# Optimization experiments

Hardware: AMD Instinct MI355X
Metric: run time of the kernel (lower is better)

## Reference

```python
import jax, jax.numpy as jnp
import numpy as np

M1 = M2 = 16      # spectral modes
CM1 = CM2 = 4     # cft modes = modes // 4
L_SEG = 4
M_CHEB = 8
PAD = 9


def _cft2d(x):
    # x: [B,C,H,W]; H,W divisible by L_SEG, segment length divisible by M_CHEB
    B, C, H, W = x.shape
    hs, ws = H // L_SEG, W // L_SEG
    seg = x.reshape(B, C, L_SEG, hs, L_SEG, ws).transpose(0, 1, 2, 4, 3, 5)
    seg = seg.reshape(B, C, L_SEG * L_SEG, hs * ws)  # row-major segment order (i,j)
    seg = seg / jnp.maximum(jnp.linalg.norm(seg, axis=-1, keepdims=True), 1e-12)
    # torch x[:,:,k::M].mean over k=0..M-1 == reshape (n//M, M), mean over rows
    coeffs = seg.reshape(B, C, L_SEG * L_SEG, (hs * ws) // M_CHEB, M_CHEB).mean(axis=3)
    coeffs = coeffs.reshape(B, C, -1)[:, :, : CM1 * CM2]
    return coeffs.reshape(B, C, CM1, CM2)  # real part; imag part is zero


def _spectral_rc(x, w1, w2, g1w, g1b, g2w, g2b):
    B, C, H, W = x.shape
    xft = jnp.fft.rfft2(x, axes=(-2, -1))
    top = jnp.einsum('bixy,ioxy->boxy', xft[:, :, :M1, :M2], w1)
    bot = jnp.einsum('bixy,ioxy->boxy', xft[:, :, H - M1:, :M2], w2)
    out_ft = jnp.zeros((B, w1.shape[1], H, W // 2 + 1), dtype=xft.dtype)
    out_ft = out_ft.at[:, :, :M1, :M2].set(top)
    out_ft = out_ft.at[:, :, H - M1:, :M2].set(bot)
    x_fno = jnp.fft.irfft2(out_ft, s=(H, W), axes=(-2, -1))
    cr = _cft2d(x)
    # torch.view_as_real interleaves (real, imag) on last axis; imag == 0
    cflat = jnp.stack([cr, jnp.zeros_like(cr)], axis=-1).reshape(B, -1)
    h = jax.nn.gelu(cflat @ g1w.T + g1b, approximate=False)
    corr = h @ g2w.T + g2b  # [B, C_out]
    return x_fno + corr[:, :, None, None]


def _forward(x, sw1r, sw1i, sw2r, sw2i, g1w, g1b, g2w, g2b, cw, cb,
             fc0w, fc0b, fc1w, fc1b, fc2w, fc2b):
    B, S1, S2, _ = x.shape
    gx = jnp.broadcast_to(jnp.linspace(0., 1., S1, dtype=x.dtype)[None, :, None, None], (B, S1, S2, 1))
    gy = jnp.broadcast_to(jnp.linspace(0., 1., S2, dtype=x.dtype)[None, None, :, None], (B, S1, S2, 1))
    h = jnp.concatenate([x, gx, gy], axis=-1) @ fc0w.T + fc0b
    h = h.transpose(0, 3, 1, 2)
    h = jnp.pad(h, ((0, 0), (0, 0), (0, PAD), (0, PAD)))
    for l in range(4):
        w1 = sw1r[l] + 1j * sw1i[l]
        w2 = sw2r[l] + 1j * sw2i[l]
        h1 = _spectral_rc(h, w1, w2, g1w[l], g1b[l], g2w[l], g2b[l])
        h2 = jnp.einsum('bchw,oc->bohw', h, cw[l]) + cb[l][None, :, None, None]
        h = h1 + h2
        if l < 3:
            h = jax.nn.gelu(h, approximate=False)
    h = h[..., :-PAD, :-PAD].transpose(0, 2, 3, 1)
    h = jax.nn.gelu(h @ fc1w.T + fc1b, approximate=False)
    return h @ fc2w.T + fc2b


def setup_inputs():
    key = jax.random.key(0)
    ks = jax.random.split(key, 20)
    B, S, Cin, Cout, Wd = 8, 119, 3, 1, 64
    f32 = jnp.float32
    scale = 1.0 / (Wd * Wd)
    return {
        'x': jax.random.normal(ks[0], (B, S, S, Cin), f32),
        'sw1r': scale * jax.random.uniform(ks[1], (4, Wd, Wd, M1, M2), f32),
        'sw1i': scale * jax.random.uniform(ks[2], (4, Wd, Wd, M1, M2), f32),
        'sw2r': scale * jax.random.uniform(ks[3], (4, Wd, Wd, M1, M2), f32),
        'sw2i': scale * jax.random.uniform(ks[4], (4, Wd, Wd, M1, M2), f32),
        'g1w': 0.02 * jax.random.normal(ks[5], (4, 256, 2048), f32),
        'g1b': 0.02 * jax.random.normal(ks[6], (4, 256), f32),
        'g2w': 0.02 * jax.random.normal(ks[7], (4, Wd, 256), f32),
        'g2b': 0.02 * jax.random.normal(ks[8], (4, Wd), f32),
        'cw': (1.0 / 8.0) * jax.random.normal(ks[9], (4, Wd, Wd), f32),
        'cb': 0.1 * jax.random.normal(ks[10], (4, Wd), f32),
        'fc0w': 0.4 * jax.random.normal(ks[11], (Wd, Cin + 2), f32),
        'fc0b': 0.1 * jax.random.normal(ks[12], (Wd,), f32),
        'fc1w': (1.0 / 8.0) * jax.random.normal(ks[13], (128, Wd), f32),
        'fc1b': 0.1 * jax.random.normal(ks[14], (128,), f32),
        'fc2w': (1.0 / 11.3) * jax.random.normal(ks[15], (Cout, 128), f32),
        'fc2b': 0.1 * jax.random.normal(ks[16], (Cout,), f32),
    }


def reference(x, sw1r, sw1i, sw2r, sw2i, g1w, g1b, g2w, g2b, cw, cb,
              fc0w, fc0b, fc1w, fc1b, fc2w, fc2b):
    return _forward(x, sw1r, sw1i, sw2r, sw2i, g1w, g1b, g2w, g2b, cw, cb,
                    fc0w, fc0b, fc1w, fc1b, fc2w, fc2b)
```

## Files before the change

### kernel.cpp

```cpp
#include <hip/hip_runtime.h>
#include <math.h>

#define NB 8
#define NC 64
#define NH 128
#define NW 128
#define NS 119
#define NPIX 113288

__device__ __forceinline__ float gelu_f(float v) {
    return 0.5f * v * (1.0f + erff(v * 0.70710678118654752f));
}

__global__ void __launch_bounds__(128) k_trig(float2* __restrict__ trig) {
    int t = threadIdx.x;
    double a = (double)t * (3.14159265358979323846 / 64.0);
    trig[t] = make_float2((float)cos(a), (float)sin(a));
}

__global__ void __launch_bounds__(128) k_tab(float2* __restrict__ wd) {
    int idx = blockIdx.x * 128 + threadIdx.x;
    int ky = idx >> 7, w = idx & 127;
    int prod = (ky * w) & 127;
    double a = (double)prod * (3.14159265358979323846 / 64.0);
    wd[idx] = make_float2((float)cos(a), (float)(-sin(a)));
}

__global__ void __launch_bounds__(256) k_tc(const float* __restrict__ fc1w,
                                            const float* __restrict__ cw,
                                            float* __restrict__ fc1wT,
                                            float* __restrict__ cwT) {
    int u = blockIdx.x * 256 + threadIdx.x;
    if (u < 8192) {
        int c = u >> 7, j = u & 127;
        fc1wT[u] = fc1w[j * 64 + c];
    } else {
        int v = u - 8192;
        int l = v >> 12, idx = v & 4095;
        int c = idx >> 6, o = idx & 63;
        cwT[v] = cw[l * 4096 + o * 64 + c];
    }
}

__global__ void __launch_bounds__(256) k_fc0(const float* __restrict__ x,
                                             const float* __restrict__ w,
                                             const float* __restrict__ bia,
                                             float* __restrict__ h) {
    __shared__ float sw[320];
    __shared__ float sb[64];
    int t = threadIdx.x;
    for (int u = t; u < 320; u += 256) sw[u] = w[u];
    if (t < 64) sb[t] = bia[t];
    __syncthreads();
    int p = blockIdx.x * 256 + t;
    int b = p >> 14;
    int rem = p & 16383;
    int r = rem >> 7, wc = rem & 127;
    float v0 = 0.f, v1 = 0.f, v2 = 0.f, gx = 0.f, gy = 0.f;
    bool inside = (r < NS) && (wc < NS);
    if (inside) {
        const float* xp = x + ((size_t)(b * NS + r) * NS + wc) * 3;
        v0 = xp[0]; v1 = xp[1]; v2 = xp[2];
        gx = (float)r * (1.0f / 118.0f);
        gy = (float)wc * (1.0f / 118.0f);
    }
    float* hp = h + (size_t)b * NC * NH * NW + rem;
    for (int c = 0; c < 64; ++c) {
        float val = 0.f;
        if (inside) {
            const float* wr = sw + c * 5;
            val = v0 * wr[0] + v1 * wr[1] + v2 * wr[2] + gx * wr[3] + gy * wr[4] + sb[c];
        }
        hp[c * (NH * NW)] = val;
    }
}

__global__ void __launch_bounds__(256) k_dft2(const float* __restrict__ h,
                                              float2* __restrict__ xft,
                                              float* __restrict__ cr,
                                              const float2* __restrict__ wd,
                                              const float2* __restrict__ trig) {
    __shared__ __align__(16) float sx[32][132];
    __shared__ __align__(16) float2 sW[16][134];
    __shared__ float2 sT[128][17];
    __shared__ float2 st[128];
    __shared__ float s_cs[2][32][8];
    __shared__ float s_cq[2][32][8];
    int t = threadIdx.x;
    int bc = blockIdx.x;
    if (t < 128) st[t] = trig[t];
    for (int u = t; u < 2048; u += 256) sW[u >> 7][u & 127] = wd[u];
    const float* src = h + (size_t)bc * 16384;
    int rp = t >> 4, ky = t & 15;
    for (int it = 0; it < 4; ++it) {
        __syncthreads();
        for (int u = t; u < 4096; u += 256) sx[u >> 7][u & 127] = src[it * 4096 + u];
        __syncthreads();
        const float* xa = sx[2 * rp];
        const float* xb = sx[2 * rp + 1];
        const float2* wk = sW[ky];
        float rea = 0.f, ima = 0.f, reb = 0.f, imb = 0.f;
#pragma unroll 8
        for (int w0 = 0; w0 < 128; w0 += 4) {
            float4 a4 = *(const float4*)(xa + w0);
            float4 b4 = *(const float4*)(xb + w0);
            float4 w01 = *(const float4*)(wk + w0);
            float4 w23 = *(const float4*)(wk + w0 + 2);
            rea += a4.x * w01.x; ima += a4.x * w01.y;
            reb += b4.x * w01.x; imb += b4.x * w01.y;
            rea += a4.y * w01.z; ima += a4.y * w01.w;
            reb += b4.y * w01.z; imb += b4.y * w01.w;
            rea += a4.z * w23.x; ima += a4.z * w23.y;
            reb += b4.z * w23.x; imb += b4.z * w23.y;
            rea += a4.w * w23.z; ima += a4.w * w23.w;
            reb += b4.w * w23.z; imb += b4.w * w23.w;
        }
        sT[it * 32 + 2 * rp][ky] = make_float2(rea, ima);
        sT[it * 32 + 2 * rp + 1][ky] = make_float2(reb, imb);
        if (it == 0) {
            int rr = t >> 3, k = t & 7;
            const float* row = sx[rr];
            float cs0 = 0.f, cq0 = 0.f, cs1 = 0.f, cq1 = 0.f;
#pragma unroll
            for (int g = 0; g < 4; ++g) {
                float a = row[g * 8 + k];       cs0 += a;  cq0 += a * a;
                float bv = row[32 + g * 8 + k]; cs1 += bv; cq1 += bv * bv;
            }
            s_cs[0][rr][k] = cs0; s_cs[1][rr][k] = cs1;
            s_cq[0][rr][k] = cq0; s_cq[1][rr][k] = cq1;
        }
    }
    __syncthreads();
    int mlo = t >> 4;
    int kxa = mlo, kxb = 112 + mlo;
    float2 sva = st[kxa]; float sca = sva.x, ssa = -sva.y;
    float2 svb = st[kxb]; float scb = svb.x, ssb = -svb.y;
    float rea = 0.f, ima = 0.f, reb = 0.f, imb = 0.f;
    for (int h0 = 0; h0 < 128; h0 += 16) {
        float2 bva = st[(kxa * h0) & 127]; float cca = bva.x, csa = -bva.y;
        float2 bvb = st[(kxb * h0) & 127]; float ccb = bvb.x, csb = -bvb.y;
#pragma unroll
        for (int j = 0; j < 16; ++j) {
            float2 Tv = sT[h0 + j][ky];
            rea += Tv.x * cca - Tv.y * csa;
            ima += Tv.x * csa + Tv.y * cca;
            reb += Tv.x * ccb - Tv.y * csb;
            imb += Tv.x * csb + Tv.y * ccb;
            float na = cca * sca - csa * ssa; csa = cca * ssa + csa * sca; cca = na;
            float nb = ccb * scb - csb * ssb; csb = ccb * ssb + csb * scb; ccb = nb;
        }
    }
    float2* xp = xft + (size_t)bc * 512;
    xp[mlo * 16 + ky] = make_float2(rea, ima);
    xp[(mlo + 16) * 16 + ky] = make_float2(reb, imb);
    if (t < 16) {
        int half = t >> 3, k = t & 7;
        float s = 0.f, q = 0.f;
        for (int rr = 0; rr < 32; ++rr) {
            s += s_cs[half][rr][k];
#pragma unroll
            for (int kk = 0; kk < 8; ++kk) q += s_cq[half][rr][kk];
        }
        float norm = fmaxf(sqrtf(q), 1e-12f);
        cr[bc * 16 + t] = s / (128.0f * norm);
    }
}

__global__ void __launch_bounds__(512) k_mixmlp(const float2* __restrict__ xft,
                                                const float* __restrict__ w1r,
                                                const float* __restrict__ w1i,
                                                const float* __restrict__ w2r,
                                                const float* __restrict__ w2i,
                                                const float* __restrict__ cr,
                                                const float* __restrict__ g1w,
                                                const float* __restrict__ g1b,
                                                float* __restrict__ hmid,
                                                float2* __restrict__ F) {
    __shared__ __align__(16) char smem[36864];
    int t = threadIdx.x;
    int bid = blockIdx.x;
    if (bid < 512) {
        float2* s_w = (float2*)smem;
        float2* s_x = (float2*)(smem + 32768);
        int m = (bid & 7) + 8 * ((bid >> 3) & 3);
        int e = bid >> 5;
        const float* wr; const float* wi; int mm;
        if (m < 16) { wr = w1r; wi = w1i; mm = m; } else { wr = w2r; wi = w2i; mm = m - 16; }
        int off = mm * 16 + e;
        for (int u = t; u < 4096; u += 512) {
            s_w[u] = make_float2(wr[(u << 8) + off], wi[(u << 8) + off]);
        }
        {
            int bb = t >> 6, i = t & 63;
            s_x[bb * 64 + i] = xft[((size_t)(bb * 64 + i) * 32 + m) * 16 + e];
        }
        __syncthreads();
        int bb = t >> 6, o = t & 63;
        float re = 0.f, im = 0.f;
#pragma unroll 8
        for (int i = 0; i < 64; ++i) {
            float2 xv = s_x[bb * 64 + i];
            float2 wv = s_w[i * 64 + o];
            re += xv.x * wv.x - xv.y * wv.y;
            im += xv.x * wv.y + xv.y * wv.x;
        }
        F[((size_t)(bb * 16 + e) * 32 + m) * 64 + o] = make_float2(re, im);
    } else {
        float* s_cr   = (float*)smem;
        float* s_wave = (float*)(smem + 32768);
        int j = bid - 512;
        for (int u = t; u < 8192; u += 512) s_cr[u] = cr[u];
        const float* wrow = g1w + (size_t)j * 2048;
        float w0 = wrow[4 * t], w1 = wrow[4 * t + 2];
        __syncthreads();
        float acc[8];
#pragma unroll
        for (int b = 0; b < 8; ++b) {
            float2 v = *(const float2*)(s_cr + b * 1024 + 2 * t);
            acc[b] = v.x * w0 + v.y * w1;
        }
#pragma unroll
        for (int d = 32; d > 0; d >>= 1) {
#pragma unroll
            for (int b = 0; b < 8; ++b) acc[b] += __shfl_down(acc[b], d, 64);
        }
        int wv = t >> 6;
        if ((t & 63) == 0) {
#pragma unroll
            for (int b = 0; b < 8; ++b) s_wave[wv * 8 + b] = acc[b];
        }
        __syncthreads();
        if (t < 8) {
            float a = g1b[j];
            for (int q = 0; q < 8; ++q) a += s_wave[q * 8 + t];
            hmid[t * 256 + j] = gelu_f(a);
        }
    }
}

__global__ void __launch_bounds__(256, 4) k_invb(const float2* __restrict__ F,
                                                 const float* __restrict__ hin,
                                                 const float* __restrict__ cwTl,
                                                 const float* __restrict__ cbl,
                                                 const float* __restrict__ hmid,
                                                 const float* __restrict__ g2w,
                                                 const float* __restrict__ g2b,
                                                 const float2* __restrict__ trig,
                                                 float* __restrict__ hout,
                                                 int do_gelu) {
    int blk = blockIdx.x;
    int b = blk >> 7, h = blk & 127;
    __shared__ __align__(16) float s_cwT[64][64];
    __shared__ __align__(16) float2 s_g[16][64];
    __shared__ float2 s_t[128];
    __shared__ float s_co[64];
    __shared__ float s_part[4][64];
    int t = threadIdx.x;
    if (t < 128) s_t[t] = trig[t];
    {
        float* cw0 = &s_cwT[0][0];
        for (int u = t; u < 4096; u += 256) cw0[u] = cwTl[u];
    }
    {
        int o = t & 63, q = t >> 6;
        const float* hv = hmid + b * 256 + q * 64;
        const float* gw = g2w + o * 256 + q * 64;
        float a = 0.f;
#pragma unroll 8
        for (int v = 0; v < 64; ++v) a += hv[v] * gw[v];
        s_part[q][o] = a;
    }
    {
        float2 rot = trig[h];
        int o = t & 63, ky0 = t >> 6;
        const float2* Fb = F + (size_t)b * 32768 + o;
        float a0r=0.f,a0i=0.f,a1r=0.f,a1i=0.f,a2r=0.f,a2i=0.f,a3r=0.f,a3i=0.f;
        float zr = 1.f, zi = 0.f;
        for (int m = 0; m < 16; ++m) {
            const float2* fm = Fb + m * 64;
            float2 f0 = fm[(ky0     ) * 2048];
            float2 f1 = fm[(ky0 +  4) * 2048];
            float2 f2 = fm[(ky0 +  8) * 2048];
            float2 f3 = fm[(ky0 + 12) * 2048];
            a0r += f0.x*zr - f0.y*zi; a0i += f0.x*zi + f0.y*zr;
            a1r += f1.x*zr - f1.y*zi; a1i += f1.x*zi + f1.y*zr;
            a2r += f2.x*zr - f2.y*zi; a2i += f2.x*zi + f2.y*zr;
            a3r += f3.x*zr - f3.y*zi; a3i += f3.x*zi + f3.y*zr;
            float nz = zr*rot.x - zi*rot.y; zi = zr*rot.y + zi*rot.x; zr = nz;
        }
        float z2r = zr, z2i = -zi;
        for (int m = 16; m < 32; ++m) {
            const float2* fm = Fb + m * 64;
            float2 f0 = fm[(ky0     ) * 2048];
            float2 f1 = fm[(ky0 +  4) * 2048];
            float2 f2 = fm[(ky0 +  8) * 2048];
            float2 f3 = fm[(ky0 + 12) * 2048];
            a0r += f0.x*z2r - f0.y*z2i; a0i += f0.x*z2i + f0.y*z2r;
            a1r += f1.x*z2r - f1.y*z2i; a1i += f1.x*z2i + f1.y*z2r;
            a2r += f2.x*z2r - f2.y*z2i; a2i += f2.x*z2i + f2.y*z2r;
            a3r += f3.x*z2r - f3.y*z2i; a3i += f3.x*z2i + f3.y*z2r;
            float nz = z2r*rot.x - z2i*rot.y; z2i = z2r*rot.y + z2i*rot.x; z2r = nz;
        }
        s_g[ky0     ][o] = make_float2(a0r, a0i);
        s_g[ky0 +  4][o] = make_float2(a1r, a1i);
        s_g[ky0 +  8][o] = make_float2(a2r, a2i);
        s_g[ky0 + 12][o] = make_float2(a3r, a3i);
    }
    __syncthreads();
    if (t < 64)
        s_co[t] = s_part[0][t] + s_part[1][t] + s_part[2][t] + s_part[3][t]
                + g2b[t] + cbl[t];
    int ot2 = t >> 6;
    int wt6 = t & 63;
    int o0 = ot2 * 16;
    float acc[16][2];
#pragma unroll
    for (int i = 0; i < 16; ++i) { acc[i][0] = 0.f; acc[i][1] = 0.f; }
    float2 rw0 = s_t[wt6];
    float2 rw1 = s_t[wt6 + 64];
    float z0r = 1.f, z0i = 0.f, z1r = 1.f, z1i = 0.f;
    const float invn = 1.0f / 16384.0f;
    for (int ky = 0; ky < 16; ++ky) {
        float fs = (ky == 0) ? invn : (2.f * invn);
        float tc0 = fs * z0r, ts0 = fs * z0i;
        float tc1 = fs * z1r, ts1 = fs * z1i;
        const float4* gk = (const float4*)(&s_g[ky][o0]);
#pragma unroll
        for (int i2 = 0; i2 < 8; ++i2) {
            float4 g2 = gk[i2];
            acc[2*i2][0]   += g2.x * tc0 - g2.y * ts0;
            acc[2*i2][1]   += g2.x * tc1 - g2.y * ts1;
            acc[2*i2+1][0] += g2.z * tc0 - g2.w * ts0;
            acc[2*i2+1][1] += g2.z * tc1 - g2.w * ts1;
        }
        float nz0 = z0r * rw0.x - z0i * rw0.y; z0i = z0r * rw0.y + z0i * rw0.x; z0r = nz0;
        float nz1 = z1r * rw1.x - z1i * rw1.y; z1i = z1r * rw1.y + z1i * rw1.x; z1r = nz1;
    }
    const float* hp = hin + ((size_t)(b * 64) * 128 + h) * 128;
    for (int cc = 0; cc < 64; cc += 4) {
        float hv0[4], hv1[4];
#pragma unroll
        for (int c = 0; c < 4; ++c) {
            hv0[c] = hp[(size_t)(cc + c) * 16384 + wt6];
            hv1[c] = hp[(size_t)(cc + c) * 16384 + wt6 + 64];
        }
#pragma unroll
        for (int c = 0; c < 4; ++c) {
            const float4* cwp = (const float4*)(&s_cwT[cc + c][o0]);
#pragma unroll
            for (int i4 = 0; i4 < 4; ++i4) {
                float4 cv = cwp[i4];
                acc[4*i4][0]   += cv.x * hv0[c]; acc[4*i4][1]   += cv.x * hv1[c];
                acc[4*i4+1][0] += cv.y * hv0[c]; acc[4*i4+1][1] += cv.y * hv1[c];
                acc[4*i4+2][0] += cv.z * hv0[c]; acc[4*i4+2][1] += cv.z * hv1[c];
                acc[4*i4+3][0] += cv.w * hv0[c]; acc[4*i4+3][1] += cv.w * hv1[c];
            }
        }
    }
    __syncthreads();
#pragma unroll
    for (int i = 0; i < 16; ++i) {
        int o = o0 + i;
        float co = s_co[o];
        float* outp = hout + ((size_t)(b * 64 + o) * 128 + h) * 128;
        float v0 = acc[i][0] + co;
        float v1 = acc[i][1] + co;
        if (do_gelu) { v0 = gelu_f(v0); v1 = gelu_f(v1); }
        outp[wt6] = v0;
        outp[wt6 + 64] = v1;
    }
}

__global__ void __launch_bounds__(256, 2) k_invbh(const float2* __restrict__ F,
                                                  const float* __restrict__ hin,
                                                  const float* __restrict__ cwTl,
                                                  const float* __restrict__ cbl,
                                                  const float* __restrict__ hmid,
                                                  const float* __restrict__ g2w,
                                                  const float* __restrict__ g2b,
                                                  const float2* __restrict__ trig,
                                                  const float* __restrict__ fc1wT,
                                                  const float* __restrict__ fc1b,
                                                  const float* __restrict__ fc2w,
                                                  const float* __restrict__ fc2b,
                                                  float* __restrict__ out) {
    int blk = blockIdx.x;
    int b = blk / 119;
    int h = blk - b * 119;
    __shared__ __align__(16) char smem[32768];
    float*  s_cwT = (float*)smem;
    float2* s_g   = (float2*)(smem + 16384);
    float*  s_hall= (float*)smem;
    __shared__ __align__(16) float s_w8[16][128];
    __shared__ float2 s_t[128];
    __shared__ float s_co[64];
    __shared__ float s_b1[128];
    __shared__ float s_w2[128];
    __shared__ float s_red[4][132];
    __shared__ float s_part[4][64];
    int t = threadIdx.x;
    if (t < 128) s_t[t] = trig[t];
    else { s_b1[t - 128] = fc1b[t - 128]; s_w2[t - 128] = fc2w[t - 128]; }
    for (int u = t; u < 4096; u += 256) s_cwT[u] = cwTl[u];
    {
        int o = t & 63, q = t >> 6;
        const float* hv = hmid + b * 256 + q * 64;
        const float* gw = g2w + o * 256 + q * 64;
        float a = 0.f;
#pragma unroll 8
        for (int v = 0; v < 64; ++v) a += hv[v] * gw[v];
        s_part[q][o] = a;
    }
    {
        float2 rot = trig[h];
        int o = t & 63, ky0 = t >> 6;
        const float2* Fb = F + (size_t)b * 32768 + o;
        float a0r=0.f,a0i=0.f,a1r=0.f,a1i=0.f,a2r=0.f,a2i=0.f,a3r=0.f,a3i=0.f;
        float zr = 1.f, zi = 0.f;
        for (int m = 0; m < 16; ++m) {
            const float2* fm = Fb + m * 64;
            float2 f0 = fm[(ky0     ) * 2048];
            float2 f1 = fm[(ky0 +  4) * 2048];
            float2 f2 = fm[(ky0 +  8) * 2048];
            float2 f3 = fm[(ky0 + 12) * 2048];
            a0r += f0.x*zr - f0.y*zi; a0i += f0.x*zi + f0.y*zr;
            a1r += f1.x*zr - f1.y*zi; a1i += f1.x*zi + f1.y*zr;
            a2r += f2.x*zr - f2.y*zi; a2i += f2.x*zi + f2.y*zr;
            a3r += f3.x*zr - f3.y*zi; a3i += f3.x*zi + f3.y*zr;
            float nz = zr*rot.x - zi*rot.y; zi = zr*rot.y + zi*rot.x; zr = nz;
        }
        float z2r = zr, z2i = -zi;
        for (int m = 16; m < 32; ++m) {
            const float2* fm = Fb + m * 64;
            float2 f0 = fm[(ky0     ) * 2048];
            float2 f1 = fm[(ky0 +  4) * 2048];
            float2 f2 = fm[(ky0 +  8) * 2048];
            float2 f3 = fm[(ky0 + 12) * 2048];
            a0r += f0.x*z2r - f0.y*z2i; a0i += f0.x*z2i + f0.y*z2r;
            a1r += f1.x*z2r - f1.y*z2i; a1i += f1.x*z2i + f1.y*z2r;
            a2r += f2.x*z2r - f2.y*z2i; a2i += f2.x*z2i + f2.y*z2r;
            a3r += f3.x*z2r - f3.y*z2i; a3i += f3.x*z2i + f3.y*z2r;
            float nz = z2r*rot.x - z2i*rot.y; z2i = z2r*rot.y + z2i*rot.x; z2r = nz;
        }
        float2* sg = (float2*)(smem + 16384);
        sg[(ky0     ) * 64 + o] = make_float2(a0r, a0i);
        sg[(ky0 +  4) * 64 + o] = make_float2(a1r, a1i);
        sg[(ky0 +  8) * 64 + o] = make_float2(a2r, a2i);
        sg[(ky0 + 12) * 64 + o] = make_float2(a3r, a3i);
    }
    __syncthreads();
    if (t < 64)
        s_co[t] = s_part[0][t] + s_part[1][t] + s_part[2][t] + s_part[3][t]
                + g2b[t] + cbl[t];
    int ot2 = t >> 6;
    int wt6 = t & 63;
    int o0 = ot2 * 16;
    float acc[16][2];
#pragma unroll
    for (int i = 0; i < 16; ++i) { acc[i][0] = 0.f; acc[i][1] = 0.f; }
    float2 rw0 = s_t[wt6];
    float2 rw1 = s_t[wt6 + 64];
    float z0r = 1.f, z0i = 0.f, z1r = 1.f, z1i = 0.f;
    const float invn = 1.0f / 16384.0f;
    for (int ky = 0; ky < 16; ++ky) {
        float fs = (ky == 0) ? invn : (2.f * invn);
        float tc0 = fs * z0r, ts0 = fs * z0i;
        float tc1 = fs * z1r, ts1 = fs * z1i;
        const float4* gk = (const float4*)(s_g + ky * 64 + o0);
#pragma unroll
        for (int i2 = 0; i2 < 8; ++i2) {
            float4 g2 = gk[i2];
            acc[2*i2][0]   += g2.x * tc0 - g2.y * ts0;
            acc[2*i2][1]   += g2.x * tc1 - g2.y * ts1;
            acc[2*i2+1][0] += g2.z * tc0 - g2.w * ts0;
            acc[2*i2+1][1] += g2.z * tc1 - g2.w * ts1;
        }
        float nz0 = z0r * rw0.x - z0i * rw0.y; z0i = z0r * rw0.y + z0i * rw0.x; z0r = nz0;
        float nz1 = z1r * rw1.x - z1i * rw1.y; z1i = z1r * rw1.y + z1i * rw1.x; z1r = nz1;
    }
    const float* hp = hin + ((size_t)(b * 64) * 128 + h) * 128;
    for (int cc = 0; cc < 64; cc += 8) {
        float hv0[8], hv1[8];
#pragma unroll
        for (int c = 0; c < 8; ++c) {
            hv0[c] = hp[(size_t)(cc + c) * 16384 + wt6];
            hv1[c] = hp[(size_t)(cc + c) * 16384 + wt6 + 64];
        }
#pragma unroll
        for (int c = 0; c < 8; ++c) {
            const float4* cwp = (const float4*)(s_cwT + (cc + c) * 64 + o0);
#pragma unroll
            for (int i4 = 0; i4 < 4; ++i4) {
                float4 cv = cwp[i4];
                acc[4*i4][0]   += cv.x * hv0[c]; acc[4*i4][1]   += cv.x * hv1[c];
                acc[4*i4+1][0] += cv.y * hv0[c]; acc[4*i4+1][1] += cv.y * hv1[c];
                acc[4*i4+2][0] += cv.z * hv0[c]; acc[4*i4+2][1] += cv.z * hv1[c];
                acc[4*i4+3][0] += cv.w * hv0[c]; acc[4*i4+3][1] += cv.w * hv1[c];
            }
        }
    }
    __syncthreads();
#pragma unroll
    for (int i = 0; i < 16; ++i) {
        float co = s_co[o0 + i];
        s_hall[(o0 + i) * 128 + wt6]      = acc[i][0] + co;
        s_hall[(o0 + i) * 128 + wt6 + 64] = acc[i][1] + co;
    }
    int j0 = ot2 * 32;
    float a32[32][2];
#pragma unroll
    for (int i = 0; i < 32; ++i) { a32[i][0] = 0.f; a32[i][1] = 0.f; }
    for (int cc = 0; cc < 64; cc += 16) {
        __syncthreads();
        for (int u = t; u < 2048; u += 256)
            s_w8[u >> 7][u & 127] = fc1wT[(cc + (u >> 7)) * 128 + (u & 127)];
        __syncthreads();
        for (int c = 0; c < 16; ++c) {
            float hv0 = s_hall[(cc + c) * 128 + wt6];
            float hv1 = s_hall[(cc + c) * 128 + wt6 + 64];
            const float4* wp = (const float4*)(&s_w8[c][j0]);
#pragma unroll
            for (int q = 0; q < 8; ++q) {
                float4 wx = wp[q];
                a32[4*q][0]   += wx.x * hv0; a32[4*q][1]   += wx.x * hv1;
                a32[4*q+1][0] += wx.y * hv0; a32[4*q+1][1] += wx.y * hv1;
                a32[4*q+2][0] += wx.z * hv0; a32[4*q+2][1] += wx.z * hv1;
                a32[4*q+3][0] += wx.w * hv0; a32[4*q+3][1] += wx.w * hv1;
            }
        }
    }
    float sum0 = 0.f, sum1 = 0.f;
#pragma unroll
    for (int i = 0; i < 32; ++i) {
        float b1 = s_b1[j0 + i];
        float w2 = s_w2[j0 + i];
        sum0 += gelu_f(a32[i][0] + b1) * w2;
        sum1 += gelu_f(a32[i][1] + b1) * w2;
    }
    s_red[ot2][wt6] = sum0;
    s_red[ot2][wt6 + 64] = sum1;
    __syncthreads();
    if (t < NS) {
        out[b * (NS * NS) + h * NS + t] =
            fc2b[0] + s_red[0][t] + s_red[1][t] + s_red[2][t] + s_red[3][t];
    }
}

extern "C" void kernel_launch(void* const* d_in, const int* in_sizes, int n_in,
                              void* d_out, int out_size, void* d_ws, size_t ws_size,
                              hipStream_t stream) {
    const float* x    = (const float*)d_in[0];
    const float* sw1r = (const float*)d_in[1];
    const float* sw1i = (const float*)d_in[2];
    const float* sw2r = (const float*)d_in[3];
    const float* sw2i = (const float*)d_in[4];
    const float* g1w  = (const float*)d_in[5];
    const float* g1b  = (const float*)d_in[6];
    const float* g2w  = (const float*)d_in[7];
    const float* g2b  = (const float*)d_in[8];
    const float* cw   = (const float*)d_in[9];
    const float* cb   = (const float*)d_in[10];
    const float* fc0w = (const float*)d_in[11];
    const float* fc0b = (const float*)d_in[12];
    const float* fc1w = (const float*)d_in[13];
    const float* fc1b = (const float*)d_in[14];
    const float* fc2w = (const float*)d_in[15];
    const float* fc2b = (const float*)d_in[16];
    float* out = (float*)d_out;

    char* ws = (char*)d_ws;
    const size_t SZ_H   = (size_t)NB * NC * NH * NW * 4;
    const size_t SZ_XFT = (size_t)NB * NC * 32 * 16 * 8;
    const size_t SZ_F   = SZ_XFT;
    size_t off = 0;
    float2* trig = (float2*)(ws + off); off += 1024;
    float2* wdft = (float2*)(ws + off); off += 2048 * 8;
    float*  f1T  = (float*)(ws + off);  off += 8192 * 4;
    float*  cwT  = (float*)(ws + off);  off += 16384 * 4;
    float*  hA   = (float*)(ws + off);  off += SZ_H;
    float*  hB   = (float*)(ws + off);  off += SZ_H;
    float2* xft  = (float2*)(ws + off); off += SZ_XFT;
    float2* F    = (float2*)(ws + off); off += SZ_F;
    float*  cr   = (float*)(ws + off);  off += (size_t)NB * NC * 16 * 4;
    float*  hmid = (float*)(ws + off);  off += (size_t)NB * 256 * 4;
    (void)ws_size; (void)in_sizes; (void)n_in; (void)out_size;

    k_trig<<<1, 128, 0, stream>>>(trig);
    k_tab<<<16, 128, 0, stream>>>(wdft);
    k_tc<<<96, 256, 0, stream>>>(fc1w, cw, f1T, cwT);
    k_fc0<<<512, 256, 0, stream>>>(x, fc0w, fc0b, hA);

    float* hcur = hA;
    float* hnxt = hB;
    for (int l = 0; l < 4; ++l) {
        const float* w1r = sw1r + (size_t)l * 1048576;
        const float* w1i = sw1i + (size_t)l * 1048576;
        const float* w2r = sw2r + (size_t)l * 1048576;
        const float* w2i = sw2i + (size_t)l * 1048576;
        const float* g1w_l = g1w + (size_t)l * 524288;
        const float* g1b_l = g1b + l * 256;
        const float* g2w_l = g2w + (size_t)l * 16384;
        const float* g2b_l = g2b + l * 64;
        const float* cwT_l = cwT + (size_t)l * 4096;
        const float* cb_l  = cb + l * 64;

        k_dft2<<<512, 256, 0, stream>>>(hcur, xft, cr, wdft, trig);
        k_mixmlp<<<768, 512, 0, stream>>>(xft, w1r, w1i, w2r, w2i,
                                          cr, g1w_l, g1b_l, hmid, F);
        if (l < 3) {
            k_invb<<<1024, 256, 0, stream>>>(F, hcur, cwT_l, cb_l, hmid,
                                             g2w_l, g2b_l, trig, hnxt, 1);
            float* tmp = hcur; hcur = hnxt; hnxt = tmp;
        } else {
            k_invbh<<<NB * NS, 256, 0, stream>>>(F, hcur, cwT_l, cb_l, hmid,
                                                 g2w_l, g2b_l, trig,
                                                 f1T, fc1b, fc2w, fc2b, out);
        }
    }
}
```

Baseline: 499.8 us.

## Compute row DFT in k_dft2 with bf16 MFMA instead of scalar FMA

Moves the first-stage row DFT (128-point input rows times a 16-mode twiddle matrix) onto 16x16x32 bf16 MFMA instructions. Each tile of activations is converted to bf16 into shared memory, and a precomputed, fragment-ordered bf16 twiddle table is held in registers. This replaces the scalar FMA inner loop and the fp32 twiddle table in shared memory. Rounding both inputs and twiddles to bf16 reduces precision and may affect tolerance. The CFT statistics now read directly from global memory.

```diff
diff --git a/kernel.cpp b/kernel.cpp
--- a/kernel.cpp
+++ b/kernel.cpp
@@ -8,8 +8,18 @@
 #define NS 119
 #define NPIX 113288
 
+typedef __attribute__((ext_vector_type(8))) short bf16x8;
+typedef __attribute__((ext_vector_type(4))) float f32x4;
+typedef __attribute__((ext_vector_type(4))) unsigned short ushort4v;
+
 __device__ __forceinline__ float gelu_f(float v) {
     return 0.5f * v * (1.0f + erff(v * 0.70710678118654752f));
+}
+
+__device__ __forceinline__ unsigned short f2bf(float x) {
+    unsigned int u = __builtin_bit_cast(unsigned int, x);
+    u += 0x7FFFu + ((u >> 16) & 1u);
+    return (unsigned short)(u >> 16);
 }
 
 __global__ void __launch_bounds__(128) k_trig(float2* __restrict__ trig) {
@@ -18,12 +28,21 @@
     trig[t] = make_float2((float)cos(a), (float)sin(a));
 }
 
-__global__ void __launch_bounds__(128) k_tab(float2* __restrict__ wd) {
-    int idx = blockIdx.x * 128 + threadIdx.x;
-    int ky = idx >> 7, w = idx & 127;
-    int prod = (ky * w) & 127;
+__global__ void __launch_bounds__(256) k_tabm(short* __restrict__ wmf) {
+    int idx = blockIdx.x * 256 + threadIdx.x;
+    int f = idx >> 9;
+    int l = (idx >> 3) & 63;
+    int e = idx & 7;
+    int ni = f >> 2, k = f & 3;
+    int w = k * 32 + (l >> 4) * 8 + e;
+    int n = ni * 16 + (l & 15);
+    int q = n >> 1;
+    int prod = (q * w) & 127;
     double a = (double)prod * (3.14159265358979323846 / 64.0);
-    wd[idx] = make_float2((float)cos(a), (float)(-sin(a)));
+    float v = (float)((n & 1) ? -sin(a) : cos(a));
+    unsigned int u = __builtin_bit_cast(unsigned int, v);
+    u += 0x7FFFu + ((u >> 16) & 1u);
+    wmf[idx] = (short)(u >> 16);
 }
 
 __global__ void __launch_bounds__(256) k_tc(const float* __restrict__ fc1w,
@@ -78,10 +97,9 @@
 __global__ void __launch_bounds__(256) k_dft2(const float* __restrict__ h,
                                               float2* __restrict__ xft,
                                               float* __restrict__ cr,
-                                              const float2* __restrict__ wd,
+                                              const short* __restrict__ wmf,
                                               const float2* __restrict__ trig) {
-    __shared__ __align__(16) float sx[32][132];
-    __shared__ __align__(16) float2 sW[16][134];
+    __shared__ __align__(16) short sxb[32][136];
     __shared__ float2 sT[128][17];
     __shared__ float2 st[128];
     __shared__ float s_cs[2][32][8];
@@ -89,48 +107,54 @@
     int t = threadIdx.x;
     int bc = blockIdx.x;
     if (t < 128) st[t] = trig[t];
-    for (int u = t; u < 2048; u += 256) sW[u >> 7][u & 127] = wd[u];
+    int lane = t & 63, wv = t >> 6;
+    int mi = wv >> 1, ni = wv & 1;
+    bf16x8 bfrag[4];
+    {
+        const short* wp = wmf + ((size_t)(ni * 4) * 64 + lane) * 8;
+#pragma unroll
+        for (int k = 0; k < 4; ++k) bfrag[k] = *(const bf16x8*)(wp + k * 512);
+    }
     const float* src = h + (size_t)bc * 16384;
-    int rp = t >> 4, ky = t & 15;
+    const short* abase = &sxb[mi * 16 + (lane & 15)][(lane >> 4) * 8];
     for (int it = 0; it < 4; ++it) {
         __syncthreads();
-        for (int u = t; u < 4096; u += 256) sx[u >> 7][u & 127] = src[it * 4096 + u];
-        __syncthreads();
-        const float* xa = sx[2 * rp];
-        const float* xb = sx[2 * rp + 1];
-        const float2* wk = sW[ky];
-        float rea = 0.f, ima = 0.f, reb = 0.f, imb = 0.f;
-#pragma unroll 8
-        for (int w0 = 0; w0 < 128; w0 += 4) {
-            float4 a4 = *(const float4*)(xa + w0);
-            float4 b4 = *(const float4*)(xb + w0);
-            float4 w01 = *(const float4*)(wk + w0);
-            float4 w23 = *(const float4*)(wk + w0 + 2);
-            rea += a4.x * w01.x; ima += a4.x * w01.y;
-            reb += b4.x * w01.x; imb += b4.x * w01.y;
-            rea += a4.y * w01.z; ima += a4.y * w01.w;
-            reb += b4.y * w01.z; imb += b4.y * w01.w;
-            rea += a4.z * w23.x; ima += a4.z * w23.y;
-            reb += b4.z * w23.x; imb += b4.z * w23.y;
-            rea += a4.w * w23.z; ima += a4.w * w23.w;
-            reb += b4.w * w23.z; imb += b4.w * w23.w;
-        }
-        sT[it * 32 + 2 * rp][ky] = make_float2(rea, ima);
-        sT[it * 32 + 2 * rp + 1][ky] = make_float2(reb, imb);
+#pragma unroll
+        for (int j = 0; j < 4; ++j) {
+            int idx4 = t + j * 256;
+            float4 v = *(const float4*)(src + (size_t)it * 4096 + (size_t)idx4 * 4);
+            ushort4v pk;
+            pk.x = f2bf(v.x); pk.y = f2bf(v.y); pk.z = f2bf(v.z); pk.w = f2bf(v.w);
+            int row = idx4 >> 5, c4 = (idx4 & 31) * 4;
+            *(ushort4v*)(&sxb[row][c4]) = pk;
+        }
         if (it == 0) {
             int rr = t >> 3, k = t & 7;
-            const float* row = sx[rr];
+            const float* rowp = src + rr * 128;
             float cs0 = 0.f, cq0 = 0.f, cs1 = 0.f, cq1 = 0.f;
 #pragma unroll
             for (int g = 0; g < 4; ++g) {
-                float a = row[g * 8 + k];       cs0 += a;  cq0 += a * a;
-                float bv = row[32 + g * 8 + k]; cs1 += bv; cq1 += bv * bv;
+                float a = rowp[g * 8 + k];       cs0 += a;  cq0 += a * a;
+                float b = rowp[32 + g * 8 + k];  cs1 += b;  cq1 += b * b;
             }
             s_cs[0][rr][k] = cs0; s_cs[1][rr][k] = cs1;
             s_cq[0][rr][k] = cq0; s_cq[1][rr][k] = cq1;
         }
+        __syncthreads();
+        f32x4 D = {0.f, 0.f, 0.f, 0.f};
+#pragma unroll
+        for (int k = 0; k < 4; ++k) {
+            bf16x8 a = *(const bf16x8*)(abase + k * 32);
+            D = __builtin_amdgcn_mfma_f32_16x16x32_bf16(a, bfrag[k], D, 0, 0, 0);
+        }
+        int row = it * 32 + mi * 16 + ((lane >> 4) << 2);
+        int col = ni * 16 + (lane & 15);
+        float* sTf = (float*)&sT[0][0];
+#pragma unroll
+        for (int r = 0; r < 4; ++r) sTf[(size_t)(row + r) * 34 + col] = D[r];
     }
     __syncthreads();
+    int ky = t & 15;
     int mlo = t >> 4;
     int kxa = mlo, kxb = 112 + mlo;
     float2 sva = st[kxa]; float sca = sva.x, ssa = -sva.y;
@@ -574,9 +598,10 @@
     const size_t SZ_F   = SZ_XFT;
     size_t off = 0;
     float2* trig = (float2*)(ws + off); off += 1024;
-    float2* wdft = (float2*)(ws + off); off += 2048 * 8;
+    short*  wmf  = (short*)(ws + off);  off += 4096 * 2;
     float*  f1T  = (float*)(ws + off);  off += 8192 * 4;
     float*  cwT  = (float*)(ws + off);  off += 16384 * 4;
+    off = (off + 255) & ~(size_t)255;
     float*  hA   = (float*)(ws + off);  off += SZ_H;
     float*  hB   = (float*)(ws + off);  off += SZ_H;
     float2* xft  = (float2*)(ws + off); off += SZ_XFT;
@@ -586,7 +611,7 @@
     (void)ws_size; (void)in_sizes; (void)n_in; (void)out_size;
 
     k_trig<<<1, 128, 0, stream>>>(trig);
-    k_tab<<<16, 128, 0, stream>>>(wdft);
+    k_tabm<<<16, 256, 0, stream>>>(wmf);
     k_tc<<<96, 256, 0, stream>>>(fc1w, cw, f1T, cwT);
     k_fc0<<<512, 256, 0, stream>>>(x, fc0w, fc0b, hA);
 
@@ -604,7 +629,7 @@
         const float* cwT_l = cwT + (size_t)l * 4096;
         const float* cb_l  = cb + l * 64;
 
-        k_dft2<<<512, 256, 0, stream>>>(hcur, xft, cr, wdft, trig);
+        k_dft2<<<512, 256, 0, stream>>>(hcur, xft, cr, wmf, trig);
         k_mixmlp<<<768, 512, 0, stream>>>(xft, w1r, w1i, w2r, w2i,
                                           cr, g1w_l, g1b_l, hmid, F);
         if (l < 3) {
```

New measurement: 455.8 us. 8.8% less time.
